# Performance work log

Measured on AMD Instinct MI355X. Metric: run time of the kernel, lower is better.

## Reference

```python
import math
import jax, jax.numpy as jnp
import numpy as np

DIM = 256
DENOM = 10000.0
MAX_LENGTH = 1000
SEQ_IN = 1024
BATCH = 32
MAX_DUR = 8


def make_encoding():
    # encoding[p, 0::2] = sin(p * div), encoding[p, 1::2] = cos(p * div)
    pos = jnp.arange(MAX_LENGTH, dtype=jnp.float32)[:, None]              # (L, 1)
    div = jnp.exp(jnp.arange(0, DIM, 2, dtype=jnp.float32) * (-math.log(DENOM) / DIM))  # (D/2,)
    sin = jnp.sin(pos * div)                                              # (L, D/2)
    cos = jnp.cos(pos * div)                                              # (L, D/2)
    return jnp.stack([sin, cos], axis=-1).reshape(MAX_LENGTH, DIM)        # interleaved


def setup_inputs() -> dict:
    key = jax.random.key(0)
    durations = jax.random.randint(key, (SEQ_IN, BATCH), 0, MAX_DUR, dtype=jnp.int32)
    encoding = make_encoding()
    return {"durations": durations, "encoding": encoding}


def reference(durations, encoding):
    # durations: (S, B) int; encoding: (L, D)
    S, B = durations.shape
    cum = jnp.cumsum(durations, axis=0)          # (S, B) exclusive-end offsets
    starts = cum - durations                     # (S, B) start offset of each token
    total = cum[-1]                              # (B,) total frames per batch element
    T_out = int(jnp.max(total))                  # pad_sequence pads to longest sequence

    frames = jnp.arange(T_out, dtype=cum.dtype)  # (T,)
    # token owning frame i: first t with cum[t] > i (skips zero-duration tokens)
    token = jax.vmap(lambda c: jnp.searchsorted(c, frames, side='right'))(cum.T)  # (B, T)
    token_c = jnp.clip(token, 0, S - 1)
    pos = frames[None, :] - jnp.take_along_axis(starts.T, token_c, axis=1)        # (B, T)
    valid = frames[None, :] < total[:, None]                                      # (B, T)

    pos = jnp.clip(pos, 0, encoding.shape[0] - 1)
    emb = encoding[pos]                                                           # (B, T, D)
    emb = jnp.where(valid[..., None], emb, jnp.zeros((), emb.dtype))
    return jnp.transpose(emb, (1, 0, 2))                                          # (T, B, D)
```

## Files before the change

### kernel.cpp

```cpp
#include <hip/hip_runtime.h>

#define SEQ   1024
#define BATCH 32
#define DIM   256

__global__ __launch_bounds__(256) void pe_fill(int* __restrict__ pos, int n) {
    int i = blockIdx.x * blockDim.x + threadIdx.x;
    if (i < n) pos[i] = -1;
}

__global__ __launch_bounds__(256) void pe_scan_scatter(const int* __restrict__ dur,
                                                       int* __restrict__ pos,
                                                       int T) {
    const int b = blockIdx.x;
    const int t = threadIdx.x;
    __shared__ int ssum[256];

    int d[4];
    const int base = (t * 4) * BATCH + b;
#pragma unroll
    for (int i = 0; i < 4; ++i) d[i] = dur[base + i * BATCH];

    ssum[t] = d[0] + d[1] + d[2] + d[3];
    __syncthreads();

    for (int off = 1; off < 256; off <<= 1) {
        int v = (t >= off) ? ssum[t - off] : 0;
        __syncthreads();
        ssum[t] += v;
        __syncthreads();
    }

    int start = (t > 0) ? ssum[t - 1] : 0;
#pragma unroll
    for (int i = 0; i < 4; ++i) {
        for (int k = 0; k < d[i]; ++k) {
            int f = start + k;
            if (f < T) pos[f * BATCH + b] = k;
        }
        start += d[i];
    }
}

__global__ __launch_bounds__(256) void pe_gather(const int* __restrict__ pos,
                                                 const float4* __restrict__ enc,
                                                 float4* __restrict__ out,
                                                 int n4) {
    int idx = blockIdx.x * blockDim.x + threadIdx.x;
    if (idx >= n4) return;
    int row = idx >> 6;
    int c   = idx & 63;
    int p   = pos[row];
    float4 v;
    if (p >= 0) {
        v = enc[p * (DIM / 4) + c];
    } else {
        v.x = 0.f; v.y = 0.f; v.z = 0.f; v.w = 0.f;
    }
    out[idx] = v;
}

extern "C" void kernel_launch(void* const* d_in, const int* in_sizes, int n_in,
                              void* d_out, int out_size, void* d_ws, size_t ws_size,
                              hipStream_t stream) {
    const int*   dur = (const int*)d_in[0];
    const float* enc = (const float*)d_in[1];
    float*       out = (float*)d_out;

    const int T     = out_size / (BATCH * DIM);
    const int nrows = T * BATCH;
    int* pos = (int*)d_ws;

    pe_fill<<<(nrows + 255) / 256, 256, 0, stream>>>(pos, nrows);
    pe_scan_scatter<<<BATCH, 256, 0, stream>>>(dur, pos, T);

    const int n4 = nrows * (DIM / 4);
    pe_gather<<<(n4 + 255) / 256, 256, 0, stream>>>(
        pos, (const float4*)enc, (float4*)out, n4);
}
```

Baseline: 130.8 us.

## Fuse pad fill into scan kernel, transpose pos layout, nontemporal grid-stride gather

Removes the separate fill kernel: the scan kernel now writes -1 padding only for frames past each batch's total, storing positions in batch-major rows so the scatter writes are contiguous per batch. The gather kernel becomes a grid-stride loop with a fixed 2048-block grid and uses nontemporal stores for the large output so it does not pollute cache. This trades one kernel launch and scattered int writes for a strided pos read in the gather and dependence on the fixed grid size.

After: 133.9 us. 2.4% more time.

```diff
diff --git a/kernel.cpp b/kernel.cpp
--- a/kernel.cpp
+++ b/kernel.cpp
@@ -4,10 +4,7 @@
 #define BATCH 32
 #define DIM   256
 
-__global__ __launch_bounds__(256) void pe_fill(int* __restrict__ pos, int n) {
-    int i = blockIdx.x * blockDim.x + threadIdx.x;
-    if (i < n) pos[i] = -1;
-}
+typedef float f4 __attribute__((ext_vector_type(4)));
 
 __global__ __launch_bounds__(256) void pe_scan_scatter(const int* __restrict__ dur,
                                                        int* __restrict__ pos,
@@ -31,50 +28,50 @@
         __syncthreads();
     }
 
+    const int total = ssum[255];
     int start = (t > 0) ? ssum[t - 1] : 0;
+    int* __restrict__ prow = pos + b * T;
+
 #pragma unroll
     for (int i = 0; i < 4; ++i) {
         for (int k = 0; k < d[i]; ++k) {
-            int f = start + k;
-            if (f < T) pos[f * BATCH + b] = k;
+            prow[start + k] = k;
         }
         start += d[i];
     }
+
+    for (int f = total + t; f < T; f += 256) prow[f] = -1;
 }
 
 __global__ __launch_bounds__(256) void pe_gather(const int* __restrict__ pos,
-                                                 const float4* __restrict__ enc,
-                                                 float4* __restrict__ out,
-                                                 int n4) {
-    int idx = blockIdx.x * blockDim.x + threadIdx.x;
-    if (idx >= n4) return;
-    int row = idx >> 6;
-    int c   = idx & 63;
-    int p   = pos[row];
-    float4 v;
-    if (p >= 0) {
-        v = enc[p * (DIM / 4) + c];
-    } else {
-        v.x = 0.f; v.y = 0.f; v.z = 0.f; v.w = 0.f;
+                                                 const f4* __restrict__ enc,
+                                                 f4* __restrict__ out,
+                                                 int T, int n4) {
+    const int stride = gridDim.x * blockDim.x;
+    for (int idx = blockIdx.x * blockDim.x + threadIdx.x; idx < n4; idx += stride) {
+        const int row = idx >> 6;
+        const int c   = idx & 63;
+        const int f   = row >> 5;
+        const int b   = row & 31;
+        const int p   = pos[b * T + f];
+        f4 v = {0.f, 0.f, 0.f, 0.f};
+        if (p >= 0) v = enc[p * (DIM / 4) + c];
+        __builtin_nontemporal_store(v, &out[idx]);
     }
-    out[idx] = v;
 }
 
 extern "C" void kernel_launch(void* const* d_in, const int* in_sizes, int n_in,
                               void* d_out, int out_size, void* d_ws, size_t ws_size,
                               hipStream_t stream) {
-    const int*   dur = (const int*)d_in[0];
-    const float* enc = (const float*)d_in[1];
-    float*       out = (float*)d_out;
+    const int* dur = (const int*)d_in[0];
+    const f4*  enc = (const f4*)d_in[1];
+    f4*        out = (f4*)d_out;
 
-    const int T     = out_size / (BATCH * DIM);
-    const int nrows = T * BATCH;
+    const int T  = out_size / (BATCH * DIM);
     int* pos = (int*)d_ws;
 
-    pe_fill<<<(nrows + 255) / 256, 256, 0, stream>>>(pos, nrows);
     pe_scan_scatter<<<BATCH, 256, 0, stream>>>(dur, pos, T);
 
-    const int n4 = nrows * (DIM / 4);
-    pe_gather<<<(n4 + 255) / 256, 256, 0, stream>>>(
-        pos, (const float4*)enc, (float4*)out, n4);
+    const int n4 = T * BATCH * (DIM / 4);
+    pe_gather<<<2048, 256, 0, stream>>>(pos, enc, out, T, n4);
 }
```
